# Kernel optimization log

Measured on AMD Instinct MI355X. Metric: run time of the kernel, lower is better.

Reference implementation:

```python
import jax, jax.numpy as jnp
import numpy as np

D = 2  # spatial dimension


def conv_contract(x, filt, k_in, k_out):
    """Equivariant convolve-then-contract for one (in,out) type pair.
    x: (B, Cin, H, W) + (D,)*k_in
    filt: (O, Cin, 3, 3) + (D,)*k_in + (D,)*k_out
    The first k_in tensor indices of the filter contract with the image's
    tensor indices (absorbed into the conv's input-feature dimension).
    Torus (periodic) padding, stride 1, as per padding='TORUS'.
    """
    B, Cin, H, W = x.shape[0], x.shape[1], x.shape[2], x.shape[3]
    O = filt.shape[0]
    din, dout = D ** k_in, D ** k_out
    # fold tensor-in components into input channels: (B, Cin*din, H, W)
    xr = jnp.moveaxis(x.reshape(B, Cin, H, W, din), -1, 2).reshape(B, Cin * din, H, W)
    # filter -> (O*dout, Cin*din, 3, 3) with matching (Cin, din) ordering
    fr = filt.reshape(O, Cin, 3, 3, din, dout)
    fr = jnp.transpose(fr, (0, 5, 1, 4, 2, 3)).reshape(O * dout, Cin * din, 3, 3)
    # periodic padding then VALID conv == TORUS padding
    xp = jnp.pad(xr, ((0, 0), (0, 0), (1, 1), (1, 1)), mode='wrap')
    out = jax.lax.conv_general_dilated(xp, fr, (1, 1), 'VALID',
                                       dimension_numbers=('NCHW', 'OIHW', 'NCHW'))
    out = jnp.moveaxis(out.reshape(B, O, dout, H, W), 2, -1)  # (B,O,H,W,dout)
    return out.reshape((B, O, H, W) + (D,) * k_out)


def setup_inputs() -> dict:
    key = jax.random.key(0)
    ks = jax.random.split(key, 11)
    B, Cin, Cout, H, W = 8, 96, 96, 128, 128
    N0, N1, N2 = 3, 4, 5  # num invariant filters for tensor order 0,1,2
    b0 = 1.0 / np.sqrt(Cin * 9)
    b1 = 1.0 / np.sqrt(Cin * 9 * D)
    inp = {
        'x_scalar': jax.random.normal(ks[0], (B, Cin, H, W), dtype=jnp.float32),
        'x_vector': jax.random.normal(ks[1], (B, Cin, H, W, D), dtype=jnp.float32),
        'f_k0': jax.random.normal(ks[2], (N0, 3, 3), dtype=jnp.float32),
        'f_k1': jax.random.normal(ks[3], (N1, 3, 3, D), dtype=jnp.float32),
        'f_k2': jax.random.normal(ks[4], (N2, 3, 3, D, D), dtype=jnp.float32),
        'w_ss': jax.random.uniform(ks[5], (Cout, Cin, N0), minval=-b0, maxval=b0),
        'w_sv': jax.random.uniform(ks[6], (Cout, Cin, N1), minval=-b0, maxval=b0),
        'w_vs': jax.random.uniform(ks[7], (Cout, Cin, N1), minval=-b1, maxval=b1),
        'w_vv': jax.random.uniform(ks[8], (Cout, Cin, N2), minval=-b1, maxval=b1),
        'b_s': jax.random.uniform(ks[9], (Cout, 1, 1), minval=-b0, maxval=b0),
        'b_v': jax.random.uniform(ks[10], (Cout, 1, 1, 1), minval=-b1, maxval=b1),
    }
    return inp


def reference(x_scalar, x_vector, f_k0, f_k1, f_k2, w_ss, w_sv, w_vs, w_vv, b_s, b_v):
    # build per-pair filters: weights (O,I,N) x invariant filters (N, 3,3, D^k...)
    f_k0 = jax.lax.stop_gradient(f_k0)
    f_k1 = jax.lax.stop_gradient(f_k1)
    f_k2 = jax.lax.stop_gradient(f_k2)
    F_ss = jnp.einsum('oin,nhw->oihw', w_ss, f_k0)        # scalar->scalar
    F_sv = jnp.einsum('oin,nhwa->oihwa', w_sv, f_k1)      # scalar->vector
    F_vs = jnp.einsum('oin,nhwa->oihwa', w_vs, f_k1)      # vector->scalar
    F_vv = jnp.einsum('oin,nhwab->oihwab', w_vv, f_k2)    # vector->vector
    # convolve each input type against each output type, contract in-tensor
    # indices, and sum contributions per output type
    out_s = conv_contract(x_scalar, F_ss, 0, 0) + conv_contract(x_vector, F_vs, 1, 0)
    out_v = conv_contract(x_scalar, F_sv, 0, 1) + conv_contract(x_vector, F_vv, 1, 1)
    # use_bias='auto': regular bias for scalars, mean-scaled bias for non-scalars
    out_s = out_s + b_s[None]
    out_v = out_v + b_v[None] * jnp.mean(out_v, axis=(2, 3), keepdims=True)
    return out_s, out_v
```

## Files before the change

kernel.cpp:

```cpp
#include <hip/hip_runtime.h>

#define HWSZ 16384
#define CIN 96
#define ICTOT 288
#define OUT_S_ELEMS (8*96*16384)
#define TILE_USH (ICTOT*32)
#define NTILES 81

typedef __attribute__((ext_vector_type(8))) short bf16x8;
typedef __attribute__((ext_vector_type(4))) float f32x4;

#define VMCNT(n) asm volatile("s_waitcnt vmcnt(" #n ")" ::: "memory")

__device__ __forceinline__ unsigned short f2bf(float f){
  unsigned int u = __float_as_uint(f);
  u += 0x7FFFu + ((u >> 16) & 1u);
  return (unsigned short)(u >> 16);
}

__device__ __forceinline__ void gload16(const unsigned short* g, const unsigned short* l){
  __builtin_amdgcn_global_load_lds(
      (const __attribute__((address_space(1))) unsigned int*)g,
      (__attribute__((address_space(3))) unsigned int*)l, 16, 0, 0);
}

__global__ void pack_w_kernel(const float* __restrict__ w_ss, const float* __restrict__ w_sv,
                              const float* __restrict__ w_vs, const float* __restrict__ w_vv,
                              const float* __restrict__ f_k0, const float* __restrict__ f_k1,
                              const float* __restrict__ f_k2, unsigned short* __restrict__ WbT){
  int idx = blockIdx.x*256 + threadIdx.x;
  if (idx >= NTILES*ICTOT*32) return;
  int j = idx / (ICTOT*32); int rem = idx - j*(ICTOT*32);
  int oc = rem >> 5, cc = rem & 31;
  int tap = j % 9, cch = j / 9;
  int ic = cch*32 + cc;
  float acc = 0.f;
  if (oc < 96){
    int o = oc;
    if (ic < CIN){
      int i = ic;
      for (int n=0;n<3;++n) acc += w_ss[(o*CIN+i)*3+n]*f_k0[n*9+tap];
    } else {
      int v = ic-CIN; int i=v>>1, a=v&1;
      for (int n=0;n<4;++n) acc += w_vs[(o*CIN+i)*4+n]*f_k1[(n*9+tap)*2+a];
    }
  } else {
    int ov = oc-96; int o=ov>>1, c=ov&1;
    if (ic < CIN){
      int i = ic;
      for (int n=0;n<4;++n) acc += w_sv[(o*CIN+i)*4+n]*f_k1[(n*9+tap)*2+c];
    } else {
      int v = ic-CIN; int i=v>>1, a=v&1;
      for (int n=0;n<5;++n) acc += w_vv[(o*CIN+i)*5+n]*f_k2[((n*9+tap)*2+a)*2+c];
    }
  }
  int cc_sw = ((((cc>>3) ^ ((oc>>1)&3)) << 3) | (cc & 7));
  WbT[(size_t)j*TILE_USH + oc*32 + cc_sw] = f2bf(acc);
}

__global__ void pack_xs_kernel(const float* __restrict__ xs, unsigned short* __restrict__ Xp,
                               float* __restrict__ Part){
  __shared__ float tile[32][65];
  __shared__ float red[8][32];
  int bid = blockIdx.x;
  int ct = bid % 3; int pt = (bid/3) & 255; int b = bid / 768;
  int p0 = pt*64, c0 = ct*32;
  int t = threadIdx.x;
  int cl = t >> 6, pl = t & 63;
  for (int kk=0; kk<8; ++kk){
    int c = kk*4 + cl;
    tile[c][pl] = xs[(size_t)(b*CIN + c0 + c)*HWSZ + p0 + pl];
  }
  __syncthreads();
  int c = t & 31, pw = t >> 5;
  float psum = 0.f;
  for (int j=0;j<8;++j){
    int p = pw*8 + j;
    float v = tile[c][p];
    psum += v;
    Xp[(size_t)(b*HWSZ + p0 + p)*ICTOT + c0 + c] = f2bf(v);
  }
  red[pw][c] = psum;
  __syncthreads();
  if (t < 32){
    float s = 0.f;
    #pragma unroll
    for (int k=0;k<8;++k) s += red[k][t];
    Part[((size_t)b*ICTOT + c0 + t)*256 + pt] = s;
  }
}

__global__ void pack_xv_kernel(const float* __restrict__ xv, unsigned short* __restrict__ Xp,
                               float* __restrict__ Part){
  __shared__ float2 tile[32][65];
  __shared__ float redx[8][32], redy[8][32];
  int bid = blockIdx.x;
  int ct = bid % 3; int pt = (bid/3) & 255; int b = bid / 768;
  int p0 = pt*64, c0 = ct*32;
  int t = threadIdx.x;
  int cl = t >> 6, pl = t & 63;
  const float2* src = (const float2*)xv;
  for (int kk=0; kk<8; ++kk){
    int c = kk*4 + cl;
    tile[c][pl] = src[(size_t)(b*CIN + c0 + c)*HWSZ + p0 + pl];
  }
  __syncthreads();
  int c = t & 31, pw = t >> 5;
  float sx = 0.f, sy = 0.f;
  for (int j=0;j<8;++j){
    int p = pw*8 + j;
    float2 v = tile[c][p];
    sx += v.x; sy += v.y;
    unsigned int u = (unsigned int)f2bf(v.x) | ((unsigned int)f2bf(v.y) << 16);
    *(unsigned int*)&Xp[(size_t)(b*HWSZ + p0 + p)*ICTOT + CIN + 2*(c0+c)] = u;
  }
  redx[pw][c] = sx; redy[pw][c] = sy;
  __syncthreads();
  if (t < 32){
    float s0 = 0.f, s1 = 0.f;
    #pragma unroll
    for (int k=0;k<8;++k){ s0 += redx[k][t]; s1 += redy[k][t]; }
    Part[((size_t)b*ICTOT + CIN + 2*(c0+t)    )*256 + pt] = s0;
    Part[((size_t)b*ICTOT + CIN + 2*(c0+t) + 1)*256 + pt] = s1;
  }
}

__global__ void reduce_part_kernel(const float* __restrict__ Part, float* __restrict__ Ssum){
  int b = blockIdx.x;
  int t = threadIdx.x;
  if (t >= ICTOT) return;
  const float* p = Part + ((size_t)b*ICTOT + t)*256;
  float s = 0.f;
  #pragma unroll 8
  for (int i=0;i<256;++i) s += p[i];
  Ssum[b*ICTOT + t] = s;
}

__global__ void mbias_kernel(const float* __restrict__ w_sv, const float* __restrict__ w_vv,
                             const float* __restrict__ f_k1, const float* __restrict__ f_k2,
                             const float* __restrict__ b_v, const float* __restrict__ Ssum,
                             float* __restrict__ MB){
  int row = blockIdx.x;
  int o = row >> 1, c = row & 1;
  int lane = threadIdx.x;
  float f1s[4], f2s[5][2];
  for (int n=0;n<4;++n){
    float s=0.f;
    for (int tap=0;tap<9;++tap) s += f_k1[(n*9+tap)*2+c];
    f1s[n]=s;
  }
  for (int n=0;n<5;++n)
    for (int a=0;a<2;++a){
      float s=0.f;
      for (int tap=0;tap<9;++tap) s += f_k2[((n*9+tap)*2+a)*2+c];
      f2s[n][a]=s;
    }
  float wv[5];
  for (int k=0;k<5;++k){
    int ic = lane + 64*k;
    float v = 0.f;
    if (ic < CIN){
      for (int n=0;n<4;++n) v += w_sv[(o*CIN+ic)*4+n]*f1s[n];
    } else if (ic < ICTOT){
      int u = ic-CIN; int i=u>>1, a=u&1;
      for (int n=0;n<5;++n) v += w_vv[(o*CIN+i)*5+n]*f2s[n][a];
    }
    wv[k] = v;
  }
  for (int b=0;b<8;++b){
    float acc = 0.f;
    for (int k=0;k<5;++k){
      int ic = lane + 64*k;
      if (ic < ICTOT) acc += wv[k]*Ssum[b*ICTOT+ic];
    }
    for (int m=1;m<64;m<<=1) acc += __shfl_xor(acc, m);
    if (lane == 0) MB[b*192+row] = b_v[o]*acc*(1.f/16384.f);
  }
}

__global__ __launch_bounds__(512,2) void conv_mfma_kernel(
    const unsigned short* __restrict__ Xp, const unsigned short* __restrict__ WbT,
    const float* __restrict__ b_s, const float* __restrict__ MB,
    float* __restrict__ out){
  __shared__ unsigned short Ash[3][1536*8];
  __shared__ unsigned short Bsh[2][2048*8];

  int bid = blockIdx.x;
  int b = bid & 7, rp = bid >> 3;
  int tid = threadIdx.x;
  int lane = tid & 63, w = tid >> 6;
  int wr = w >> 2, wc = w & 3;
  int cl = lane & 15, g = lane >> 4;

  f32x4 acc[9][4];
  #pragma unroll
  for (int m=0;m<9;++m)
    #pragma unroll
    for (int n=0;n<4;++n) acc[m][n] = (f32x4){0.f,0.f,0.f,0.f};

  const size_t xb = (size_t)b * HWSZ * ICTOT;
  const unsigned short* srcB[4];
  #pragma unroll
  for (int i=0;i<4;++i){
    int f = i*512 + tid;
    int j = f >> 9, px = (f >> 2) & 127, cp = f & 3;
    int cps = cp ^ ((px >> 1) & 3);
    int hs = (2*rp - 1 + j + 128) & 127;
    srcB[i] = Xp + xb + ((size_t)(hs*128 + px))*ICTOT + cps*8;
  }
  const unsigned short* srcA = WbT + tid*8;
  const int wlds = w*64*8;
  const int Abase = (wr*144 + cl)*32 + ((g ^ ((cl>>1)&3))*8);
  const int pxb = (wc & 1)*64 + cl;
  const int jr0 = (wc >> 1);

  int boff[3][4];
  #pragma unroll
  for (int kx=0;kx<3;++kx)
    #pragma unroll
    for (int n=0;n<4;++n){
      int px = (pxb + n*16 + kx + 127) & 127;
      boff[kx][n] = px*32 + ((g ^ ((px >> 1) & 3))*8);
    }

  #pragma unroll
  for (int i=0;i<4;++i) gload16(srcB[i], &Bsh[0][i*512*8 + wlds]);
  #pragma unroll
  for (int i=0;i<3;++i) gload16(srcA + 0*TILE_USH + i*4096, &Ash[0][i*512*8 + wlds]);
  #pragma unroll
  for (int i=0;i<3;++i) gload16(srcA + 1*TILE_USH + i*4096, &Ash[1][i*512*8 + wlds]);
  VMCNT(3);
  __builtin_amdgcn_s_barrier();

  const unsigned short* cA = srcA;
  for (int c = 0; c < 9; ++c){
    const unsigned short* Bcur = Bsh[c & 1];
    unsigned short* Bnxt = (unsigned short*)Bsh[(c & 1) ^ 1];
    #pragma unroll
    for (int t = 0; t < 9; ++t){
      if (c < 8 || t <= 6){
        #pragma unroll
        for (int i=0;i<3;++i)
          gload16(cA + (t+2)*TILE_USH + i*4096, &Ash[(t+2)%3][i*512*8 + wlds]);
      }
      if (t == 0 && c < 8){
        #pragma unroll
        for (int i=0;i<4;++i)
          gload16(srcB[i] + (c+1)*32, &Bnxt[i*512*8 + wlds]);
      }
      const int ky = t / 3, kx = t % 3;
      const unsigned short* Bj = Bcur + (jr0 + ky)*4096;
      bf16x8 bfr[4];
      #pragma unroll
      for (int n=0;n<4;++n) bfr[n] = *(const bf16x8*)&Bj[boff[kx][n]];
      const unsigned short* At = Ash[t % 3];
      __builtin_amdgcn_s_setprio(1);
      #pragma unroll
      for (int m=0;m<9;++m){
        bf16x8 af = *(const bf16x8*)&At[Abase + m*512];
        #pragma unroll
        for (int n=0;n<4;++n)
          acc[m][n] = __builtin_amdgcn_mfma_f32_16x16x32_bf16(af, bfr[n], acc[m][n], 0,0,0);
      }
      __builtin_amdgcn_s_setprio(0);
      if (t <= 1){ if (c < 8) { VMCNT(7); } else { VMCNT(3); } }
      else if (t >= 7){ if (c == 8) { VMCNT(0); } else { VMCNT(3); } }
      else { VMCNT(3); }
      __builtin_amdgcn_sched_barrier(0);
      __builtin_amdgcn_s_barrier();
    }
    cA += 9*TILE_USH;
  }

  const int orow = 2*rp + (wc >> 1);
  const int colb = (wc & 1)*64;
  #pragma unroll
  for (int m=0;m<9;++m){
    int ocb = wr*144 + m*16 + 4*g;
    if (wr == 0 && m < 6){
      #pragma unroll
      for (int r=0;r<4;++r){
        int oc = ocb + r;
        float bias = b_s[oc];
        #pragma unroll
        for (int n=0;n<4;++n){
          int p = orow*128 + colb + n*16 + cl;
          out[(size_t)(b*96+oc)*HWSZ + p] = acc[m][n][r] + bias;
        }
      }
    } else {
      float2* outv = (float2*)(out + OUT_S_ELEMS);
      int row0 = ocb - 96;
      int o0 = row0 >> 1;
      float mb0 = MB[b*192+row0  ], mb1 = MB[b*192+row0+1];
      float mb2 = MB[b*192+row0+2], mb3 = MB[b*192+row0+3];
      #pragma unroll
      for (int n=0;n<4;++n){
        int p = orow*128 + colb + n*16 + cl;
        outv[(size_t)(b*96+o0  )*HWSZ + p] = (float2){acc[m][n][0]+mb0, acc[m][n][1]+mb1};
        outv[(size_t)(b*96+o0+1)*HWSZ + p] = (float2){acc[m][n][2]+mb2, acc[m][n][3]+mb3};
      }
    }
  }
}

extern "C" void kernel_launch(void* const* d_in, const int* in_sizes, int n_in,
                              void* d_out, int out_size, void* d_ws, size_t ws_size,
                              hipStream_t stream){
  const float* xs   = (const float*)d_in[0];
  const float* xv   = (const float*)d_in[1];
  const float* f_k0 = (const float*)d_in[2];
  const float* f_k1 = (const float*)d_in[3];
  const float* f_k2 = (const float*)d_in[4];
  const float* w_ss = (const float*)d_in[5];
  const float* w_sv = (const float*)d_in[6];
  const float* w_vs = (const float*)d_in[7];
  const float* w_vv = (const float*)d_in[8];
  const float* b_s  = (const float*)d_in[9];
  const float* b_v  = (const float*)d_in[10];
  float* out = (float*)d_out;

  char* ws = (char*)d_ws;
  unsigned short* WbT = (unsigned short*)ws;
  const size_t XP_OFF = (size_t)NTILES*TILE_USH*2 + 6144;
  unsigned short* Xp = (unsigned short*)(ws + XP_OFF);
  const size_t PART_OFF = XP_OFF + (size_t)8*HWSZ*ICTOT*2;
  float* Part = (float*)(ws + PART_OFF);
  float* Ssum = (float*)(ws + PART_OFF + 2359296);
  float* MB   = (float*)(ws + PART_OFF + 2359296 + 9216);

  pack_w_kernel<<<(NTILES*ICTOT*32 + 255)/256, 256, 0, stream>>>(
      w_ss, w_sv, w_vs, w_vv, f_k0, f_k1, f_k2, WbT);
  pack_xs_kernel<<<6144, 256, 0, stream>>>(xs, Xp, Part);
  pack_xv_kernel<<<6144, 256, 0, stream>>>(xv, Xp, Part);
  reduce_part_kernel<<<8, 320, 0, stream>>>(Part, Ssum);
  mbias_kernel<<<192, 64, 0, stream>>>(w_sv, w_vv, f_k1, f_k2, b_v, Ssum, MB);
  conv_mfma_kernel<<<512, 512, 0, stream>>>(Xp, WbT, b_s, MB, out);
}
```

Before: 257.1 us.

## Prefetch next tap's LDS fragments into registers and merge input pack kernels

The MFMA main loop now reads the A and B fragments for the next tap from LDS into registers after the wait and before the barrier. The MFMAs for the current tap then run on operands already held in registers, so LDS read latency no longer stalls the matrix cores. The two input-packing kernels are merged into one launch with a block-index branch, removing one kernel launch. Costs are higher register pressure from 13 live fragment vectors, a full VMCNT(0) in the prologue, and reworked wait counts whose correctness depends on the prefetch order.

```diff
diff --git a/kernel.cpp b/kernel.cpp
--- a/kernel.cpp
+++ b/kernel.cpp
@@ -58,70 +58,68 @@
   WbT[(size_t)j*TILE_USH + oc*32 + cc_sw] = f2bf(acc);
 }
 
-__global__ void pack_xs_kernel(const float* __restrict__ xs, unsigned short* __restrict__ Xp,
-                               float* __restrict__ Part){
-  __shared__ float tile[32][65];
-  __shared__ float red[8][32];
-  int bid = blockIdx.x;
-  int ct = bid % 3; int pt = (bid/3) & 255; int b = bid / 768;
-  int p0 = pt*64, c0 = ct*32;
+__global__ void pack_x_kernel(const float* __restrict__ xs, const float* __restrict__ xv,
+                              unsigned short* __restrict__ Xp, float* __restrict__ Part){
+  __shared__ float2 tile[32][65];
+  __shared__ float red[2][8][32];
+  int bid0 = blockIdx.x;
   int t = threadIdx.x;
-  int cl = t >> 6, pl = t & 63;
-  for (int kk=0; kk<8; ++kk){
-    int c = kk*4 + cl;
-    tile[c][pl] = xs[(size_t)(b*CIN + c0 + c)*HWSZ + p0 + pl];
-  }
-  __syncthreads();
-  int c = t & 31, pw = t >> 5;
-  float psum = 0.f;
-  for (int j=0;j<8;++j){
-    int p = pw*8 + j;
-    float v = tile[c][p];
-    psum += v;
-    Xp[(size_t)(b*HWSZ + p0 + p)*ICTOT + c0 + c] = f2bf(v);
-  }
-  red[pw][c] = psum;
-  __syncthreads();
-  if (t < 32){
-    float s = 0.f;
-    #pragma unroll
-    for (int k=0;k<8;++k) s += red[k][t];
-    Part[((size_t)b*ICTOT + c0 + t)*256 + pt] = s;
-  }
-}
-
-__global__ void pack_xv_kernel(const float* __restrict__ xv, unsigned short* __restrict__ Xp,
-                               float* __restrict__ Part){
-  __shared__ float2 tile[32][65];
-  __shared__ float redx[8][32], redy[8][32];
-  int bid = blockIdx.x;
-  int ct = bid % 3; int pt = (bid/3) & 255; int b = bid / 768;
-  int p0 = pt*64, c0 = ct*32;
-  int t = threadIdx.x;
-  int cl = t >> 6, pl = t & 63;
-  const float2* src = (const float2*)xv;
-  for (int kk=0; kk<8; ++kk){
-    int c = kk*4 + cl;
-    tile[c][pl] = src[(size_t)(b*CIN + c0 + c)*HWSZ + p0 + pl];
-  }
-  __syncthreads();
-  int c = t & 31, pw = t >> 5;
-  float sx = 0.f, sy = 0.f;
-  for (int j=0;j<8;++j){
-    int p = pw*8 + j;
-    float2 v = tile[c][p];
-    sx += v.x; sy += v.y;
-    unsigned int u = (unsigned int)f2bf(v.x) | ((unsigned int)f2bf(v.y) << 16);
-    *(unsigned int*)&Xp[(size_t)(b*HWSZ + p0 + p)*ICTOT + CIN + 2*(c0+c)] = u;
-  }
-  redx[pw][c] = sx; redy[pw][c] = sy;
-  __syncthreads();
-  if (t < 32){
-    float s0 = 0.f, s1 = 0.f;
-    #pragma unroll
-    for (int k=0;k<8;++k){ s0 += redx[k][t]; s1 += redy[k][t]; }
-    Part[((size_t)b*ICTOT + CIN + 2*(c0+t)    )*256 + pt] = s0;
-    Part[((size_t)b*ICTOT + CIN + 2*(c0+t) + 1)*256 + pt] = s1;
+  if (bid0 < 6144){
+    int bid = bid0;
+    int ct = bid % 3; int pt = (bid/3) & 255; int b = bid / 768;
+    int p0 = pt*64, c0 = ct*32;
+    float* tf = (float*)tile;
+    int cl = t >> 6, pl = t & 63;
+    for (int kk=0; kk<8; ++kk){
+      int c = kk*4 + cl;
+      tf[c*130 + pl] = xs[(size_t)(b*CIN + c0 + c)*HWSZ + p0 + pl];
+    }
+    __syncthreads();
+    int c = t & 31, pw = t >> 5;
+    float psum = 0.f;
+    for (int j=0;j<8;++j){
+      int p = pw*8 + j;
+      float v = tf[c*130 + p];
+      psum += v;
+      Xp[(size_t)(b*HWSZ + p0 + p)*ICTOT + c0 + c] = f2bf(v);
+    }
+    red[0][pw][c] = psum;
+    __syncthreads();
+    if (t < 32){
+      float s = 0.f;
+      #pragma unroll
+      for (int k=0;k<8;++k) s += red[0][k][t];
+      Part[((size_t)b*ICTOT + c0 + t)*256 + pt] = s;
+    }
+  } else {
+    int bid = bid0 - 6144;
+    int ct = bid % 3; int pt = (bid/3) & 255; int b = bid / 768;
+    int p0 = pt*64, c0 = ct*32;
+    int cl = t >> 6, pl = t & 63;
+    const float2* src = (const float2*)xv;
+    for (int kk=0; kk<8; ++kk){
+      int c = kk*4 + cl;
+      tile[c][pl] = src[(size_t)(b*CIN + c0 + c)*HWSZ + p0 + pl];
+    }
+    __syncthreads();
+    int c = t & 31, pw = t >> 5;
+    float sx = 0.f, sy = 0.f;
+    for (int j=0;j<8;++j){
+      int p = pw*8 + j;
+      float2 v = tile[c][p];
+      sx += v.x; sy += v.y;
+      unsigned int u = (unsigned int)f2bf(v.x) | ((unsigned int)f2bf(v.y) << 16);
+      *(unsigned int*)&Xp[(size_t)(b*HWSZ + p0 + p)*ICTOT + CIN + 2*(c0+c)] = u;
+    }
+    red[0][pw][c] = sx; red[1][pw][c] = sy;
+    __syncthreads();
+    if (t < 32){
+      float s0 = 0.f, s1 = 0.f;
+      #pragma unroll
+      for (int k=0;k<8;++k){ s0 += red[0][k][t]; s1 += red[1][k][t]; }
+      Part[((size_t)b*ICTOT + CIN + 2*(c0+t)    )*256 + pt] = s0;
+      Part[((size_t)b*ICTOT + CIN + 2*(c0+t) + 1)*256 + pt] = s1;
+    }
   }
 }
 
@@ -224,13 +222,19 @@
     }
 
   #pragma unroll
-  for (int i=0;i<4;++i) gload16(srcB[i], &Bsh[0][i*512*8 + wlds]);
-  #pragma unroll
-  for (int i=0;i<3;++i) gload16(srcA + 0*TILE_USH + i*4096, &Ash[0][i*512*8 + wlds]);
-  #pragma unroll
-  for (int i=0;i<3;++i) gload16(srcA + 1*TILE_USH + i*4096, &Ash[1][i*512*8 + wlds]);
-  VMCNT(3);
+  for (int i=0;i<4;++i) gload16(srcB[i], &Bsh[0][i*4096 + wlds]);
+  #pragma unroll
+  for (int i=0;i<3;++i) gload16(srcA + 0*TILE_USH + i*4096, &Ash[0][i*4096 + wlds]);
+  #pragma unroll
+  for (int i=0;i<3;++i) gload16(srcA + 1*TILE_USH + i*4096, &Ash[1][i*4096 + wlds]);
+  VMCNT(0);
   __builtin_amdgcn_s_barrier();
+
+  bf16x8 afc[9], bfc[4];
+  #pragma unroll
+  for (int n=0;n<4;++n) bfc[n] = *(const bf16x8*)&Bsh[0][jr0*4096 + boff[0][n]];
+  #pragma unroll
+  for (int m=0;m<9;++m) afc[m] = *(const bf16x8*)&Ash[0][Abase + m*512];
 
   const unsigned short* cA = srcA;
   for (int c = 0; c < 9; ++c){
@@ -241,31 +245,33 @@
       if (c < 8 || t <= 6){
         #pragma unroll
         for (int i=0;i<3;++i)
-          gload16(cA + (t+2)*TILE_USH + i*4096, &Ash[(t+2)%3][i*512*8 + wlds]);
+          gload16(cA + (t+2)*TILE_USH + i*4096, &Ash[(t+2)%3][i*4096 + wlds]);
       }
       if (t == 0 && c < 8){
         #pragma unroll
         for (int i=0;i<4;++i)
-          gload16(srcB[i] + (c+1)*32, &Bnxt[i*512*8 + wlds]);
-      }
-      const int ky = t / 3, kx = t % 3;
-      const unsigned short* Bj = Bcur + (jr0 + ky)*4096;
-      bf16x8 bfr[4];
-      #pragma unroll
-      for (int n=0;n<4;++n) bfr[n] = *(const bf16x8*)&Bj[boff[kx][n]];
-      const unsigned short* At = Ash[t % 3];
+          gload16(srcB[i] + (c+1)*32, &Bnxt[i*4096 + wlds]);
+      }
       __builtin_amdgcn_s_setprio(1);
       #pragma unroll
       for (int m=0;m<9;++m){
-        bf16x8 af = *(const bf16x8*)&At[Abase + m*512];
         #pragma unroll
         for (int n=0;n<4;++n)
-          acc[m][n] = __builtin_amdgcn_mfma_f32_16x16x32_bf16(af, bfr[n], acc[m][n], 0,0,0);
+          acc[m][n] = __builtin_amdgcn_mfma_f32_16x16x32_bf16(afc[m], bfc[n], acc[m][n], 0,0,0);
       }
       __builtin_amdgcn_s_setprio(0);
-      if (t <= 1){ if (c < 8) { VMCNT(7); } else { VMCNT(3); } }
-      else if (t >= 7){ if (c == 8) { VMCNT(0); } else { VMCNT(3); } }
-      else { VMCNT(3); }
+      if (c < 8){ if (t <= 1) { VMCNT(7); } else { VMCNT(3); } }
+      else      { if (t <= 6) { VMCNT(3); } else if (t == 7) { VMCNT(0); } }
+      if (c < 8 || t < 8){
+        const int tau = (t+1)%9;
+        const int ky = tau/3, kx = tau%3;
+        const unsigned short* Bsrc = (t < 8 ? Bcur : (const unsigned short*)Bnxt) + (jr0 + ky)*4096;
+        #pragma unroll
+        for (int n=0;n<4;++n) bfc[n] = *(const bf16x8*)&Bsrc[boff[kx][n]];
+        const unsigned short* At = Ash[(t+1)%3];
+        #pragma unroll
+        for (int m=0;m<9;++m) afc[m] = *(const bf16x8*)&At[Abase + m*512];
+      }
       __builtin_amdgcn_sched_barrier(0);
       __builtin_amdgcn_s_barrier();
     }
@@ -331,8 +337,7 @@
 
   pack_w_kernel<<<(NTILES*ICTOT*32 + 255)/256, 256, 0, stream>>>(
       w_ss, w_sv, w_vs, w_vv, f_k0, f_k1, f_k2, WbT);
-  pack_xs_kernel<<<6144, 256, 0, stream>>>(xs, Xp, Part);
-  pack_xv_kernel<<<6144, 256, 0, stream>>>(xv, Xp, Part);
+  pack_x_kernel<<<12288, 256, 0, stream>>>(xs, xv, Xp, Part);
   reduce_part_kernel<<<8, 320, 0, stream>>>(Part, Ssum);
   mbias_kernel<<<192, 64, 0, stream>>>(w_sv, w_vv, f_k1, f_k2, b_v, Ssum, MB);
   conv_mfma_kernel<<<512, 512, 0, stream>>>(Xp, WbT, b_s, MB, out);
```

Result: faster. 240.0 us (-6.6%).
